# Optimization experiments

Measured on AMD Instinct MI355X. Metric: run time of the kernel, lower is better.

Reference implementation:

```python
import jax, jax.numpy as jnp
import numpy as np
from jax import lax

B, T, IDIM, HDIM = 128, 256, 64, 128
TS, KS, OC1, ANF = 64, 3, 100, 64
S1 = TS - 3 * (KS - 1)   # 58: three VALID ks=3 stride-1 convs
S = S1 * S1              # 3364
HN = 2 * HDIM            # 256 = h_dim * l_dim (l_dim=2)
F = S + HN               # 3620
HID = F // 2             # 1810


def _conv(x, w, b):
    y = lax.conv_general_dilated(x, w, (1, 1), 'VALID',
                                 dimension_numbers=('NCHW', 'OIHW', 'NCHW'))
    return y + b[None, :, None, None]


def _lstm_layer(x, w_ih, w_hh, b_ih, b_hh):
    # x: [B, T, D] -> (outputs [B, T, H], final hidden [B, H]); PyTorch gate order i,f,g,o
    Bn = x.shape[0]
    h0 = jnp.zeros((Bn, HDIM), x.dtype)
    c0 = jnp.zeros((Bn, HDIM), x.dtype)
    def step(carry, xt):
        h, c = carry
        g = xt @ w_ih.T + h @ w_hh.T + b_ih + b_hh
        i, f, gg, o = jnp.split(g, 4, axis=-1)
        c = jax.nn.sigmoid(f) * c + jax.nn.sigmoid(i) * jnp.tanh(gg)
        h = jax.nn.sigmoid(o) * jnp.tanh(c)
        return (h, c), h
    (hT, cT), ys = lax.scan(step, (h0, c0), jnp.swapaxes(x, 0, 1))
    return jnp.swapaxes(ys, 0, 1), hT


def setup_inputs() -> dict:
    key = jax.random.key(0)
    k = jax.random.split(key, 30)
    s = 0.05
    H4 = 4 * HDIM
    return {
        'x1': jax.random.normal(k[0], (B, 3, TS, TS), jnp.float32),
        'x2': jax.random.normal(k[1], (B, T, IDIM), jnp.float32),
        # conv2a/conv2b: two Monte-Carlo weight samples of the same Bayesian conv2 layer
        'conv1_w': jax.random.normal(k[2], (OC1, 3, KS, KS), jnp.float32) * s,
        'conv1_b': jax.random.normal(k[3], (OC1,), jnp.float32) * s,
        'conv2a_w': jax.random.normal(k[4], (OC1, OC1, KS, KS), jnp.float32) * s,
        'conv2a_b': jax.random.normal(k[5], (OC1,), jnp.float32) * s,
        'conv2b_w': jax.random.normal(k[6], (OC1, OC1, KS, KS), jnp.float32) * s,
        'conv2b_b': jax.random.normal(k[7], (OC1,), jnp.float32) * s,
        'w_ih0': jax.random.normal(k[8], (H4, IDIM), jnp.float32) * s,
        'w_hh0': jax.random.normal(k[9], (H4, HDIM), jnp.float32) * s,
        'b_ih0': jax.random.normal(k[10], (H4,), jnp.float32) * s,
        'b_hh0': jax.random.normal(k[11], (H4,), jnp.float32) * s,
        'w_ih1': jax.random.normal(k[12], (H4, HDIM), jnp.float32) * s,
        'w_hh1': jax.random.normal(k[13], (H4, HDIM), jnp.float32) * s,
        'b_ih1': jax.random.normal(k[14], (H4,), jnp.float32) * s,
        'b_hh1': jax.random.normal(k[15], (H4,), jnp.float32) * s,
        'attn1_w': jax.random.normal(k[16], (ANF, F), jnp.float32) * s,
        'attn1_b': jax.random.normal(k[17], (ANF,), jnp.float32) * s,
        'attn2_w': jax.random.normal(k[18], (1, ANF), jnp.float32) * s,
        'attn2_b': jax.random.normal(k[19], (1,), jnp.float32) * s,
        'fc1_w': jax.random.normal(k[20], (HID, F), jnp.float32) * s,
        'fc1_b': jax.random.normal(k[21], (HID,), jnp.float32) * s,
        'fc2_w': jax.random.normal(k[22], (1, HID), jnp.float32) * s,
        'fc2_b': jax.random.normal(k[23], (1,), jnp.float32) * s,
    }


def reference(x1, x2, conv1_w, conv1_b, conv2a_w, conv2a_b, conv2b_w, conv2b_b,
              w_ih0, w_hh0, b_ih0, b_hh0, w_ih1, w_hh1, b_ih1, b_hh1,
              attn1_w, attn1_b, attn2_w, attn2_b, fc1_w, fc1_b, fc2_w, fc2_b):
    Bn = x1.shape[0]
    # CNN branch
    x = jax.nn.relu(_conv(x1, conv1_w, conv1_b))
    x = jax.nn.relu(_conv(x, conv2a_w, conv2a_b))
    x = jax.nn.relu(_conv(x, conv2b_w, conv2b_b))
    xd = x.reshape(Bn, OC1, S)                               # [B, oc1, S]
    # LSTM branch (2 layers, dropout in eval mode = identity)
    y0, h0f = _lstm_layer(x2, w_ih0, w_hh0, b_ih0, b_hh0)
    _, h1f = _lstm_layer(y0, w_ih1, w_hh1, b_ih1, b_hh1)
    hn = jnp.concatenate([h0f, h1f], axis=1)                 # [B, 2*h_dim]
    # Broadcast hidden state across channels (replaces the torch concat loop)
    hn_b = jnp.broadcast_to(hn[:, None, :], (Bn, OC1, HN))
    fused = jnp.concatenate([xd, hn_b], axis=2)              # [B, oc1, F]
    # Attention
    a = jnp.tanh(fused @ attn1_w.T + attn1_b)                # [B, oc1, anf]
    a = a @ attn2_w.T + attn2_b                              # [B, oc1, 1]
    a = jax.nn.softmax(a, axis=1)
    ctx = jnp.einsum('bcs,bco->bso', xd, a).reshape(Bn, S)   # [B, S]
    # Fusion MLP (dropout eval-mode identity)
    m = jnp.concatenate([ctx, hn], axis=1)                   # [B, F]
    h = jax.nn.relu(m @ fc1_w.T + fc1_b)
    return h @ fc2_w.T + fc2_b                               # [B, 1]
```

## Files before the change

kernel.cpp:

```cpp
#include <hip/hip_runtime.h>
#include <hip/hip_bf16.h>
#include <math.h>

#define BB 128
#define TT 256
#define IDIM 64
#define HD 128
#define G4 512
#define OC 100
#define W1 62
#define W2 60
#define W3 58
#define NPX1 (W1*W1)
#define NPX2 (W2*W2)
#define NPX3 (W3*W3)
#define SS NPX3
#define FF (SS + 2*HD)
#define HIDN 1810
#define ANF 64
#define ROWSPLIT 47

typedef __hip_bfloat16 bf16;
typedef _Float16 f16;
typedef __attribute__((ext_vector_type(8))) short bf16x8;
typedef __attribute__((ext_vector_type(4))) short bf16x4;
typedef __attribute__((ext_vector_type(2))) _Float16 half2v;
typedef __attribute__((ext_vector_type(4))) float f32x4;

__device__ __forceinline__ float ldf(const float* p) { return *p; }
__device__ __forceinline__ float ldf(const bf16* p)  { return __bfloat162float(*p); }
__device__ __forceinline__ void  stf(float* p, float v) { *p = v; }
__device__ __forceinline__ void  stf(bf16* p, float v)  { *p = __float2bfloat16(v); }

__device__ __forceinline__ short f2bs(float v) {
    bf16 t = __float2bfloat16(v); short s; __builtin_memcpy(&s, &t, 2); return s;
}
__device__ __forceinline__ float fsig(float x) {
    return __builtin_amdgcn_rcpf(1.f + __expf(-x));
}
__device__ __forceinline__ float ftanh(float x) {
    float t = __expf(-2.f * fabsf(x));
    float r = __builtin_amdgcn_rcpf(1.f + t);
    float m = 1.f - 2.f * t * r;
    return copysignf(m, x);
}
__device__ __forceinline__ float fmix2(unsigned w, unsigned h, float acc) {
    half2v wv, hv;
    __builtin_memcpy(&wv, &w, 4);
    __builtin_memcpy(&hv, &h, 4);
    acc = fmaf((float)wv[0], (float)hv[0], acc);
    acc = fmaf((float)wv[1], (float)hv[1], acc);
    return acc;
}

__device__ __forceinline__ bf16x8 load8(const bf16* p) { return *(const bf16x8*)p; }
__device__ __forceinline__ bf16x8 load8(const float* p) {
    float4 x = *(const float4*)p;
    float4 y = *(const float4*)(p + 4);
    bf16x8 r;
    r[0] = f2bs(x.x); r[1] = f2bs(x.y); r[2] = f2bs(x.z); r[3] = f2bs(x.w);
    r[4] = f2bs(y.x); r[5] = f2bs(y.y); r[6] = f2bs(y.z); r[7] = f2bs(y.w);
    return r;
}

__global__ void zero_kernel(float* o, int n)
{
    int i = blockIdx.x * 256 + threadIdx.x;
    if (i < n) o[i] = 0.f;
}

__device__ __forceinline__ void body_cvt_bf16(const float* __restrict__ s, bf16* __restrict__ d,
                                              int i, int n4)
{
    if (i >= n4) return;
    float4 v = ((const float4*)s)[i];
    bf16x4 o;
    o[0] = f2bs(v.x); o[1] = f2bs(v.y); o[2] = f2bs(v.z); o[3] = f2bs(v.w);
    *(bf16x4*)(d + 4 * (size_t)i) = o;
}
__device__ __forceinline__ void body_cvt_f16(const float* __restrict__ s, f16* __restrict__ d,
                                             int i, int n4)
{
    if (i >= n4) return;
    float4 v = ((const float4*)s)[i];
    f16 o[4] = {(f16)v.x, (f16)v.y, (f16)v.z, (f16)v.w};
    *(uint2*)(d + 4 * (size_t)i) = *(uint2*)o;
}
__device__ __forceinline__ void body_wt(const float* __restrict__ w, bf16* __restrict__ WT, int idx)
{
    if (idx >= 129024) return;
    int i  = idx & 31;
    int oc = (idx >> 5) % 112;
    int ts = idx / (112 * 32);
    int s = ts & 3, t = ts >> 2;
    int ic = s * 32 + i;
    float v = 0.f;
    if (oc < OC && ic < OC) v = w[(oc * OC + ic) * 9 + t];
    WT[idx] = __float2bfloat16(v);
}

__global__ __launch_bounds__(256)
void prep_kernel(const float* __restrict__ x2,   bf16* __restrict__ X2B,
                 const float* __restrict__ whh0, f16*  __restrict__ LWf0,
                 const float* __restrict__ whh1, f16*  __restrict__ LWf1,
                 const float* __restrict__ wih0, bf16* __restrict__ WIH0B,
                 const float* __restrict__ wih1, bf16* __restrict__ WIH1B,
                 const float* __restrict__ a1w,  bf16* __restrict__ A1WB,
                 const float* __restrict__ bih0, const float* __restrict__ bhh0, float* __restrict__ BS0,
                 const float* __restrict__ bih1, const float* __restrict__ bhh1, float* __restrict__ BS1,
                 const float* __restrict__ c2aw, bf16* __restrict__ WTa,
                 const float* __restrict__ c2bw, bf16* __restrict__ WTb)
{
    int bid = blockIdx.x;
    int tid = threadIdx.x;
    if (bid < 2048)      body_cvt_bf16(x2,   X2B,   bid * 256 + tid, 524288);
    else if (bid < 2112) body_cvt_f16 (whh0, LWf0, (bid - 2048) * 256 + tid, 16384);
    else if (bid < 2176) body_cvt_f16 (whh1, LWf1, (bid - 2112) * 256 + tid, 16384);
    else if (bid < 2208) body_cvt_bf16(wih0, WIH0B, (bid - 2176) * 256 + tid, 8192);
    else if (bid < 2272) body_cvt_bf16(wih1, WIH1B, (bid - 2208) * 256 + tid, 16384);
    else if (bid < 2499) body_cvt_bf16(a1w,  A1WB,  (bid - 2272) * 256 + tid, 57920);
    else if (bid < 2500) { BS0[tid] = bih0[tid] + bhh0[tid]; BS0[tid + 256] = bih0[tid + 256] + bhh0[tid + 256]; }
    else if (bid < 2501) { BS1[tid] = bih1[tid] + bhh1[tid]; BS1[tid + 256] = bih1[tid + 256] + bhh1[tid + 256]; }
    else if (bid < 3005) body_wt(c2aw, WTa, (bid - 2501) * 256 + tid);
    else                 body_wt(c2bw, WTb, (bid - 3005) * 256 + tid);
}

__device__ __forceinline__
void conv1_body(const float* __restrict__ x1, const float* __restrict__ wl,
                const float* __restrict__ bl, bf16* __restrict__ out, int b, int py, int t)
{
    int px = py * 256 + t;
    if (px >= NPX1) return;
    int y = px / W1, x = px % W1;
    float in[3][3][3];
    const float* xb = x1 + (size_t)b * 3 * 64 * 64;
#pragma unroll
    for (int ic = 0; ic < 3; ic++)
#pragma unroll
        for (int r = 0; r < 3; r++)
#pragma unroll
            for (int c = 0; c < 3; c++)
                in[ic][r][c] = xb[(ic * 64 + y + r) * 64 + x + c];
    bf16* ob = out + (size_t)b * OC * NPX1 + px;
    for (int oc = 0; oc < OC; ++oc) {
        float acc = bl[oc];
        const float* wp = &wl[oc * 27];
#pragma unroll
        for (int ic = 0; ic < 3; ic++)
#pragma unroll
            for (int r = 0; r < 3; r++)
#pragma unroll
                for (int c = 0; c < 3; c++)
                    acc = fmaf(in[ic][r][c], wp[ic * 9 + r * 3 + c], acc);
        ob[(size_t)oc * NPX1] = __float2bfloat16(fmaxf(acc, 0.f));
    }
}

__global__ __launch_bounds__(256)
void conv1_kernel(const float* __restrict__ x1, const float* __restrict__ w,
                  const float* __restrict__ bias, bf16* __restrict__ out)
{
    __shared__ float wl[2700];
    __shared__ float bl[OC];
    int tid = threadIdx.x;
    for (int i = tid; i < 2700; i += 256) wl[i] = w[i];
    if (tid < OC) bl[tid] = bias[tid];
    __syncthreads();
    conv1_body(x1, wl, bl, out, blockIdx.x, blockIdx.y, tid);
}

__device__ __forceinline__
void conv2_body(const bf16* __restrict__ in, const bf16* __restrict__ WT,
                const float* __restrict__ bias, bf16* __restrict__ out,
                int iw, int ow, int b, int yblk, int tid,
                bf16* __restrict__ il, bf16* __restrict__ wl)
{
    int y0 = yblk * 8;
    int wid = tid >> 6;
    int l = tid & 63;
    int hq = l >> 4;
    int l16 = l & 15;
    int yo = y0 + wid;

    f32x4 acc[7][4];
#pragma unroll
    for (int f = 0; f < 7; f++) {
#pragma unroll
        for (int r = 0; r < 4; r++) {
            int oc = f * 16 + hq * 4 + r;
            float bv = (oc < OC) ? bias[oc] : 0.f;
#pragma unroll
            for (int n = 0; n < 4; n++) acc[f][n][r] = bv;
        }
    }

    const size_t ims = (size_t)iw * iw;
    int icl = tid & 31;
    int t2  = tid >> 5;
    for (int s = 0; s < 4; ++s) {
        __syncthreads();
        int ic = s * 32 + icl;
        bool icok = ic < OC;
        const bf16* ibase = in + (size_t)(b * OC + ic) * ims;
#pragma unroll
        for (int it = 0; it < 6; ++it) {
            int u2 = t2 + it * 16;
            if (u2 < 90) {
                int r = u2 / 9, xb = u2 - r * 9;
                int x8 = xb * 8;
                int yy = y0 + r;
                bf16x8 v = {0, 0, 0, 0, 0, 0, 0, 0};
                if (icok && yy < iw && x8 < iw) {
                    const short* sp = (const short*)(ibase + (size_t)yy * iw + x8);
                    if (x8 + 8 <= iw) {
                        const unsigned* sp32 = (const unsigned*)sp;
#pragma unroll
                        for (int q = 0; q < 4; q++)
                            ((unsigned*)&v)[q] = sp32[q];
                    } else {
                        for (int k = 0; k < 8; k++)
                            if (x8 + k < iw) ((short*)&v)[k] = sp[k];
                    }
                }
                bf16* dst = &il[(r * 72 + x8) * 40 + icl];
#pragma unroll
                for (int k = 0; k < 8; k++)
                    *(short*)&dst[k * 40] = ((short*)&v)[k];
            }
        }
#pragma unroll
        for (int it = 0; it < 8; ++it) {
            int u = tid + it * 512;
            if (u < 4032) {
                int tf = u >> 6; int lp = u & 63;
                int t = tf / 7, f = tf - t * 7;
                int oc = f * 16 + (lp & 15);
                int hq2 = lp >> 4;
                *(bf16x8*)&wl[(size_t)u * 8] =
                    *(const bf16x8*)(WT + (size_t)((t * 4 + s) * 112 + oc) * 32 + hq2 * 8);
            }
        }
        __syncthreads();

#pragma unroll
        for (int ky = 0; ky < 3; ++ky) {
#pragma unroll
            for (int kx = 0; kx < 3; ++kx) {
                int t = ky * 3 + kx;
                bf16x8 a[7];
#pragma unroll
                for (int f = 0; f < 7; f++)
                    a[f] = *(const bf16x8*)&wl[(size_t)((t * 7 + f) * 64 + l) * 8];
                bf16x8 bfr[4];
#pragma unroll
                for (int n = 0; n < 4; n++)
                    bfr[n] = *(const bf16x8*)&il[((wid + ky) * 72 + kx + l16 + n * 16) * 40 + hq * 8];
#pragma unroll
                for (int f = 0; f < 7; f++)
#pragma unroll
                    for (int n = 0; n < 4; n++)
                        acc[f][n] = __builtin_amdgcn_mfma_f32_16x16x32_bf16(
                            a[f], bfr[n], acc[f][n], 0, 0, 0);
            }
        }
    }

    if (yo < ow) {
#pragma unroll
        for (int f = 0; f < 7; f++) {
#pragma unroll
            for (int r = 0; r < 4; r++) {
                int oc = f * 16 + hq * 4 + r;
                if (oc < OC) {
#pragma unroll
                    for (int n = 0; n < 4; n++) {
                        int x = n * 16 + l16;
                        if (x < ow)
                            out[((size_t)(b * OC + oc) * ow + yo) * ow + x] =
                                __float2bfloat16(fmaxf(acc[f][n][r], 0.f));
                    }
                }
            }
        }
    }
}

__global__ __launch_bounds__(512, 1)
void conv2_mfma(const bf16* __restrict__ in, const bf16* __restrict__ WT,
                const float* __restrict__ bias, bf16* __restrict__ out,
                int iw, int ow, int brow0)
{
    __shared__ bf16 il[10 * 72 * 40];
    __shared__ bf16 wl[4032 * 8];
    conv2_body(in, WT, bias, out, iw, ow, brow0 + blockIdx.x, blockIdx.y, threadIdx.x, il, wl);
}

__device__ __forceinline__
void lstm_body(const bf16* __restrict__ G, const f16* __restrict__ LWr,
               bf16* __restrict__ Y, float* __restrict__ HN, int hoff,
               int b, int g, f16* __restrict__ hl, float* __restrict__ ex)
{
    uint4 wv[16];
    const uint4* wp = (const uint4*)(LWr + (size_t)g * HD);
#pragma unroll
    for (int q = 0; q < 16; q++) wv[q] = wp[q];
#pragma unroll
    for (int q = 0; q < 16; q++)
        asm volatile("" : "+v"(wv[q].x), "+v"(wv[q].y), "+v"(wv[q].z), "+v"(wv[q].w));
    float c = 0.f;
    if (g < HD) hl[g] = (f16)0.f;
    __syncthreads();
    const bf16* Gb = G + (size_t)b * TT * G4 + g;
    float gcur = __bfloat162float(Gb[0]);
    for (int t = 0; t < TT; ++t) {
        int tn = (t + 1 < TT) ? t + 1 : t;
        bf16 gnext = Gb[(size_t)tn * G4];
        float a0 = 0.f, a1 = 0.f, a2 = 0.f, a3 = 0.f;
#pragma unroll
        for (int q = 0; q < 16; q++) {
            uint4 hw = *(const uint4*)&hl[q * 8];
            a0 = fmix2(wv[q].x, hw.x, a0);
            a1 = fmix2(wv[q].y, hw.y, a1);
            a2 = fmix2(wv[q].z, hw.z, a2);
            a3 = fmix2(wv[q].w, hw.w, a3);
        }
        float dot = gcur + (a0 + a1) + (a2 + a3);
        float tr;
        if (g < 2 * HD || g >= 3 * HD) tr = fsig(dot);
        else tr = ftanh(dot);
        ex[g] = tr;
        gcur = __bfloat162float(gnext);
        __syncthreads();
        if (g < HD) {
            float iv = ex[g], fv = ex[HD + g], gv = ex[2 * HD + g], ov = ex[3 * HD + g];
            c = fv * c + iv * gv;
            float nh = ov * ftanh(c);
            hl[g] = (f16)nh;
            if (Y) Y[((size_t)b * TT + t) * HD + g] = __float2bfloat16(nh);
            if (t == TT - 1) HN[(size_t)b * 256 + hoff + g] = nh;
        }
        __syncthreads();
    }
}

__global__ __launch_bounds__(512, 1)
void lstm_recur(const bf16* __restrict__ G, const f16* __restrict__ LWr,
                bf16* __restrict__ Y, float* __restrict__ HN, int hoff)
{
    __shared__ __align__(16) f16 hl[HD];
    __shared__ float ex[G4];
    lstm_body(G, LWr, Y, HN, hoff, blockIdx.x, threadIdx.x, hl, ex);
}

__global__ __launch_bounds__(512, 1)
void hybrid_l0c1(const bf16* __restrict__ G, const f16* __restrict__ LWf0,
                 bf16* __restrict__ Y0, float* __restrict__ HN,
                 const float* __restrict__ x1, const float* __restrict__ c1w,
                 const float* __restrict__ c1b, bf16* __restrict__ A1)
{
    __shared__ __align__(16) char smem[11264];
    int bid = blockIdx.x;
    if (bid < BB) {
        lstm_body(G, LWf0, Y0, HN, 0, bid, threadIdx.x,
                  (f16*)smem, (float*)(smem + 512));
    } else {
        float* wl = (float*)smem;
        float* bl = (float*)(smem + 10800);
        int tid = threadIdx.x;
        for (int i = tid; i < 2700; i += 512) wl[i] = c1w[i];
        if (tid < OC) bl[tid] = c1b[tid];
        __syncthreads();
        int v = (bid - BB) * 2 + (tid >> 8);
        conv1_body(x1, wl, bl, A1, v >> 4, v & 15, tid & 255);
    }
}

__global__ __launch_bounds__(512, 1)
void hybrid_l1c2a(const bf16* __restrict__ G, const f16* __restrict__ LWf1,
                  float* __restrict__ HN,
                  const bf16* __restrict__ A1, const bf16* __restrict__ WTa,
                  const float* __restrict__ c2ab, bf16* __restrict__ A2)
{
    __shared__ __align__(16) char smem[122112];
    int bid = blockIdx.x;
    if (bid < BB) {
        lstm_body(G, LWf1, (bf16*)nullptr, HN, HD, bid, threadIdx.x,
                  (f16*)smem, (float*)(smem + 512));
    } else {
        int r = bid - BB;
        conv2_body(A1, WTa, c2ab, A2, W1, W2, ROWSPLIT + (r >> 3), r & 7,
                   threadIdx.x, (bf16*)smem, (bf16*)(smem + 57600));
    }
}

template<typename TB, typename TC, int ACT>
__global__ __launch_bounds__(256)
void gemm_mfma(const bf16* __restrict__ A, int lda,
               const TB* __restrict__ B, int ldb,
               const float* __restrict__ bias,
               TC* __restrict__ C, int ldc,
               int M, int N, int K)
{
    __shared__ bf16 As[64 * 72];
    __shared__ bf16 Bs[64 * 72];
    int tid = threadIdx.x;
    int l = tid & 63, wid = tid >> 6;
    int l16 = l & 15, h = l >> 4;
    int m0 = blockIdx.x * 64, n0 = blockIdx.y * 64;
    f32x4 acc[4];
#pragma unroll
    for (int nb = 0; nb < 4; nb++) acc[nb] = (f32x4){0.f, 0.f, 0.f, 0.f};

    int rs = tid >> 3;
    int kc = (tid & 7) * 8;

    for (int k0 = 0; k0 < K; k0 += 64) {
        int kr = K - k0;
#pragma unroll
        for (int half = 0; half < 2; half++) {
            int rr = rs + half * 32;
            bf16x8 av = {0, 0, 0, 0, 0, 0, 0, 0};
            int m = m0 + rr;
            if (m < M) {
                const short* src = (const short*)(A + (size_t)m * lda + k0 + kc);
                if (kc + 8 <= kr) av = *(const bf16x8*)src;
                else if (kc < kr) {
                    for (int j = 0; j < 8; j++) if (kc + j < kr) ((short*)&av)[j] = src[j];
                }
            }
            *(bf16x8*)&As[rr * 72 + kc] = av;
            bf16x8 bv = {0, 0, 0, 0, 0, 0, 0, 0};
            int n = n0 + rr;
            if (n < N) {
                const TB* src = B + (size_t)n * ldb + k0 + kc;
                if (kc + 8 <= kr) bv = load8(src);
                else if (kc < kr) {
                    for (int j = 0; j < 8; j++) if (kc + j < kr) ((short*)&bv)[j] = f2bs(ldf(src + j));
                }
            }
            *(bf16x8*)&Bs[rr * 72 + kc] = bv;
        }
        __syncthreads();
#pragma unroll
        for (int kk = 0; kk < 2; kk++) {
            bf16x8 af = *(const bf16x8*)&As[(wid * 16 + l16) * 72 + kk * 32 + h * 8];
#pragma unroll
            for (int nb = 0; nb < 4; nb++) {
                bf16x8 bfr = *(const bf16x8*)&Bs[(nb * 16 + l16) * 72 + kk * 32 + h * 8];
                acc[nb] = __builtin_amdgcn_mfma_f32_16x16x32_bf16(af, bfr, acc[nb], 0, 0, 0);
            }
        }
        __syncthreads();
    }
#pragma unroll
    for (int nb = 0; nb < 4; nb++) {
        int col = n0 + nb * 16 + l16;
        if (col >= N) continue;
        float bv = bias ? bias[col] : 0.f;
#pragma unroll
        for (int reg = 0; reg < 4; reg++) {
            int row = m0 + wid * 16 + h * 4 + reg;
            if (row < M) {
                float v = acc[nb][reg] + bv;
                if (ACT == 1) v = fmaxf(v, 0.f);
                stf(&C[(size_t)row * ldc + col], v);
            }
        }
    }
}

template<typename TA, typename TC, int BM, int BN, int BK, int TM, int TN, int ACT>
__global__ __launch_bounds__((BM / TM) * (BN / TN))
void gemm_tn(const TA* __restrict__ A, int lda,
             const float* __restrict__ Bmat, int ldb,
             const float* __restrict__ bias,
             TC* __restrict__ C, int ldc,
             int M, int N, int K)
{
    constexpr int TX = BN / TN;
    constexpr int TY = BM / TM;
    constexpr int NT = TX * TY;
    __shared__ float As[BK][BM + 1];
    __shared__ float Bs[BK][BN + 1];
    int tid = threadIdx.x;
    int tx = tid % TX, ty = tid / TX;
    int m0 = blockIdx.x * BM, n0 = blockIdx.y * BN;
    float acc[TM][TN] = {};
    for (int k0 = 0; k0 < K; k0 += BK) {
        for (int idx = tid; idx < BM * BK; idx += NT) {
            int i = idx / BK, j = idx % BK;
            int m = m0 + i, k = k0 + j;
            As[j][i] = (m < M && k < K) ? ldf(&A[(size_t)m * lda + k]) : 0.f;
        }
        for (int idx = tid; idx < BN * BK; idx += NT) {
            int i = idx / BK, j = idx % BK;
            int n = n0 + i, k = k0 + j;
            Bs[j][i] = (n < N && k < K) ? Bmat[(size_t)n * ldb + k] : 0.f;
        }
        __syncthreads();
#pragma unroll
        for (int k = 0; k < BK; ++k) {
            float av[TM], bv[TN];
#pragma unroll
            for (int i = 0; i < TM; i++) av[i] = As[k][ty * TM + i];
#pragma unroll
            for (int j = 0; j < TN; j++) bv[j] = Bs[k][tx * TN + j];
#pragma unroll
            for (int i = 0; i < TM; i++)
#pragma unroll
                for (int j = 0; j < TN; j++)
                    acc[i][j] += av[i] * bv[j];
        }
        __syncthreads();
    }
#pragma unroll
    for (int i = 0; i < TM; i++) {
        int m = m0 + ty * TM + i;
        if (m >= M) continue;
#pragma unroll
        for (int j = 0; j < TN; j++) {
            int n = n0 + tx * TN + j;
            if (n >= N) continue;
            float v = acc[i][j] + (bias ? bias[n] : 0.f);
            if (ACT == 1) v = fmaxf(v, 0.f);
            stf(&C[(size_t)m * ldc + n], v);
        }
    }
}

__global__ __launch_bounds__(128)
void attn_softmax(const float* __restrict__ T1,
                  const float* __restrict__ HB,
                  const float* __restrict__ a2w,
                  const float* __restrict__ a2b,
                  float* __restrict__ ATT)
{
    __shared__ float hbl[ANF];
    __shared__ float awl[ANF];
    __shared__ float red[128];
    int b = blockIdx.x, tid = threadIdx.x;
    if (tid < ANF) { hbl[tid] = HB[b * ANF + tid]; awl[tid] = a2w[tid]; }
    __syncthreads();
    float lg = -1e30f;
    if (tid < OC) {
        const float* tp = T1 + (size_t)(b * OC + tid) * ANF;
        float s = 0.f;
#pragma unroll 4
        for (int j = 0; j < ANF; j++) s += ftanh(tp[j] + hbl[j]) * awl[j];
        lg = s + a2b[0];
    }
    red[tid] = lg; __syncthreads();
    for (int st = 64; st > 0; st >>= 1) { if (tid < st) red[tid] = fmaxf(red[tid], red[tid + st]); __syncthreads(); }
    float mx = red[0]; __syncthreads();
    float e = (tid < OC) ? __expf(lg - mx) : 0.f;
    red[tid] = e; __syncthreads();
    for (int st = 64; st > 0; st >>= 1) { if (tid < st) red[tid] += red[tid + st]; __syncthreads(); }
    if (tid < OC) ATT[b * OC + tid] = e / red[0];
}

__global__ __launch_bounds__(256)
void ctx_concat(const bf16* __restrict__ XD,
                const float* __restrict__ ATT,
                const float* __restrict__ HN,
                bf16* __restrict__ M)
{
    __shared__ float al[OC];
    int b = blockIdx.x;
    int tid = threadIdx.x;
    if (tid < OC) al[tid] = ATT[b * OC + tid];
    __syncthreads();
    int s = blockIdx.y * 256 + tid;
    if (s < SS) {
        const bf16* xp = XD + (size_t)b * OC * SS + s;
        float acc = 0.f;
#pragma unroll 4
        for (int c = 0; c < OC; c++) acc = fmaf(__bfloat162float(xp[(size_t)c * SS]), al[c], acc);
        M[(size_t)b * FF + s] = __float2bfloat16(acc);
    } else if (s < FF) {
        M[(size_t)b * FF + s] = __float2bfloat16(HN[b * 256 + (s - SS)]);
    }
}

__global__ __launch_bounds__(256)
void fc2_kernel(const float* __restrict__ H1, const float* __restrict__ w,
                const float* __restrict__ bias, float* __restrict__ out)
{
    int tid = threadIdx.x;
    int lane = tid & 63, wid = tid >> 6;
    int b = blockIdx.x * 4 + wid;
    float acc = 0.f;
    for (int j = lane; j < HIDN; j += 64) acc = fmaf(H1[(size_t)b * HIDN + j], w[j], acc);
#pragma unroll
    for (int off = 32; off > 0; off >>= 1) acc += __shfl_down(acc, off, 64);
    if (lane == 0) out[b] = acc + bias[0];
}

extern "C" void kernel_launch(void* const* d_in, const int* in_sizes, int n_in,
                              void* d_out, int out_size, void* d_ws, size_t ws_size,
                              hipStream_t stream)
{
    const float* x1   = (const float*)d_in[0];
    const float* x2   = (const float*)d_in[1];
    const float* c1w  = (const float*)d_in[2];
    const float* c1b  = (const float*)d_in[3];
    const float* c2aw = (const float*)d_in[4];
    const float* c2ab = (const float*)d_in[5];
    const float* c2bw = (const float*)d_in[6];
    const float* c2bb = (const float*)d_in[7];
    const float* wih0 = (const float*)d_in[8];
    const float* whh0 = (const float*)d_in[9];
    const float* bih0 = (const float*)d_in[10];
    const float* bhh0 = (const float*)d_in[11];
    const float* wih1 = (const float*)d_in[12];
    const float* whh1 = (const float*)d_in[13];
    const float* bih1 = (const float*)d_in[14];
    const float* bhh1 = (const float*)d_in[15];
    const float* a1w  = (const float*)d_in[16];
    const float* a1b  = (const float*)d_in[17];
    const float* a2w  = (const float*)d_in[18];
    const float* a2b  = (const float*)d_in[19];
    const float* f1w  = (const float*)d_in[20];
    const float* f1b  = (const float*)d_in[21];
    const float* f2w  = (const float*)d_in[22];
    const float* f2b  = (const float*)d_in[23];
    float* out = (float*)d_out;

    char* base = (char*)d_ws;
    bf16* G0    = (bf16*)(base + 0);
    bf16* Y0    = (bf16*)(base + 33554432);
    bf16* G1    = G0;
    bf16* X2B   = (bf16*)(base + 41943040);
    bf16* WIH0B = (bf16*)(base + 46137344);
    bf16* WIH1B = (bf16*)(base + 46202880);
    const size_t LSTM_END = 46333952;

    int nb = 0; size_t ov = 0;
    for (int cand = BB; cand >= 32; cand >>= 1) {
        size_t cnn = (size_t)cand * OC * (NPX1 + NPX2) * 2;
        size_t o = cnn > LSTM_END ? cnn : LSTM_END;
        size_t q = o + 2048 + 2048 + 131072 + 32768
                 + (size_t)cand * OC * 64 * 4
                 + (((size_t)cand * OC * 4 + 255) & ~(size_t)255)
                 + 926720 + 926720 + 258048 + 258048 + 463360
                 + 262144;
        if (ws_size >= q) { nb = cand; ov = o; break; }
    }
    if (nb == 0) {
        zero_kernel<<<1, 128, 0, stream>>>(out, out_size);
        return;
    }
    bf16* A1c;
    bf16* A2c;
    if (nb == BB) {
        A2c = (bf16*)(base + 0);
        A1c = (bf16*)(base + (size_t)BB * OC * NPX2 * 2);
    } else {
        A1c = (bf16*)(base + 0);
        A2c = (bf16*)(base + (size_t)nb * OC * NPX1 * 2);
    }
    bf16* XDc = A1c;
    size_t p = ov;
    float* BS0  = (float*)(base + p); p += 2048;
    float* BS1  = (float*)(base + p); p += 2048;
    float* HN   = (float*)(base + p); p += 131072;
    float* HB   = (float*)(base + p); p += 32768;
    float* T1c  = (float*)(base + p); p += (size_t)nb * OC * 64 * 4;
    float* ATTc = (float*)(base + p); p += ((size_t)nb * OC * 4 + 255) & ~(size_t)255;
    bf16*  MBb  = (bf16*)(base + p); p += 926720;
    float* H1   = (float*)(base + p); p += 926720;
    bf16* WTa   = (bf16*)(base + p); p += 258048;
    bf16* WTb   = (bf16*)(base + p); p += 258048;
    bf16* A1WB  = (bf16*)(base + p); p += 463360;
    f16*  LWf0  = (f16*)(base + p); p += 131072;
    f16*  LWf1  = (f16*)(base + p); p += 131072;

    prep_kernel<<<3509, 256, 0, stream>>>(
        x2, X2B, whh0, LWf0, whh1, LWf1, wih0, WIH0B, wih1, WIH1B, a1w, A1WB,
        bih0, bhh0, BS0, bih1, bhh1, BS1, c2aw, WTa, c2bw, WTb);

    gemm_mfma<bf16, bf16, 0><<<dim3(512, 8), 256, 0, stream>>>(
        X2B, IDIM, WIH0B, IDIM, BS0, G0, G4, BB * TT, G4, IDIM);

    if (nb == BB) {
        hybrid_l0c1<<<BB + BB * 8, 512, 0, stream>>>(
            G0, LWf0, Y0, HN, x1, c1w, c1b, A1c);
        gemm_mfma<bf16, bf16, 0><<<dim3(512, 8), 256, 0, stream>>>(
            Y0, HD, WIH1B, HD, BS1, G1, G4, BB * TT, G4, HD);
        hybrid_l1c2a<<<BB + (BB - ROWSPLIT) * 8, 512, 0, stream>>>(
            G1, LWf1, HN, A1c, WTa, c2ab, A2c);
        conv2_mfma<<<dim3(ROWSPLIT, 8), 512, 0, stream>>>(A1c, WTa, c2ab, A2c, W1, W2, 0);
        conv2_mfma<<<dim3(BB, 8), 512, 0, stream>>>(A2c, WTb, c2bb, XDc, W2, W3, 0);
        gemm_tn<float, float, 32, 32, 16, 2, 2, 0><<<dim3(4, 2), 256, 0, stream>>>(
            HN, 256, a1w + SS, FF, a1b, HB, ANF, BB, ANF, 256);
        gemm_mfma<bf16, float, 0><<<dim3(BB * OC / 64, 1), 256, 0, stream>>>(
            XDc, SS, A1WB, FF, nullptr, T1c, ANF, BB * OC, ANF, SS);
        attn_softmax<<<BB, 128, 0, stream>>>(T1c, HB, a2w, a2b, ATTc);
        ctx_concat<<<dim3(BB, 15), 256, 0, stream>>>(XDc, ATTc, HN, MBb);
    } else {
        lstm_recur<<<BB, 512, 0, stream>>>(G0, LWf0, Y0, HN, 0);
        gemm_mfma<bf16, bf16, 0><<<dim3(512, 8), 256, 0, stream>>>(
            Y0, HD, WIH1B, HD, BS1, G1, G4, BB * TT, G4, HD);
        lstm_recur<<<BB, 512, 0, stream>>>(G1, LWf1, (bf16*)nullptr, HN, HD);
        gemm_tn<float, float, 32, 32, 16, 2, 2, 0><<<dim3(4, 2), 256, 0, stream>>>(
            HN, 256, a1w + SS, FF, a1b, HB, ANF, BB, ANF, 256);
        for (int c0 = 0; c0 < BB; c0 += nb) {
            conv1_kernel<<<dim3(nb, 16), 256, 0, stream>>>(
                x1 + (size_t)c0 * 3 * 64 * 64, c1w, c1b, A1c);
            conv2_mfma<<<dim3(nb, 8), 512, 0, stream>>>(A1c, WTa, c2ab, A2c, W1, W2, 0);
            conv2_mfma<<<dim3(nb, 8), 512, 0, stream>>>(A2c, WTb, c2bb, XDc, W2, W3, 0);
            gemm_mfma<bf16, float, 0><<<dim3(nb * OC / 64, 1), 256, 0, stream>>>(
                XDc, SS, A1WB, FF, nullptr, T1c, ANF, nb * OC, ANF, SS);
            attn_softmax<<<nb, 128, 0, stream>>>(T1c, HB + (size_t)c0 * ANF, a2w, a2b, ATTc);
            ctx_concat<<<dim3(nb, 15), 256, 0, stream>>>(
                XDc, ATTc, HN + (size_t)c0 * 256, MBb + (size_t)c0 * FF);
        }
    }

    gemm_mfma<float, float, 1><<<dim3(2, 29), 256, 0, stream>>>(
        MBb, FF, f1w, FF, f1b, H1, HIDN, BB, HIDN, FF);
    fc2_kernel<<<BB / 4, 256, 0, stream>>>(H1, f2w, f2b, out);
}
```

Measured before the change: 1.058 ms.

## Restructure LSTM recurrence to one thread per hidden unit with LDS-resident gate weights

The LSTM step now uses 128 active threads per block, each computing all four gates for its hidden unit. The i-gate weights stay in registers and the f, g and o weights sit in padded LDS. A double-buffered h vector leaves one barrier per timestep instead of two, and the gate exchange through shared memory is gone. The conv2a work carried inside the hybrid layer-1 kernel is shrunk, and the remaining batches run in an extra conv2 launch. In exchange, 384 of 512 threads sit idle, each active thread does four times the dot-product work with heavy LDS weight reads, and the hybrid kernels need much more shared memory.

```diff
diff --git a/kernel.cpp b/kernel.cpp
--- a/kernel.cpp
+++ b/kernel.cpp
@@ -19,6 +19,7 @@
 #define HIDN 1810
 #define ANF 64
 #define ROWSPLIT 47
+#define HEND 104
 
 typedef __hip_bfloat16 bf16;
 typedef _Float16 f16;
@@ -296,48 +297,66 @@
 }
 
 __device__ __forceinline__
-void lstm_body(const bf16* __restrict__ G, const f16* __restrict__ LWr,
-               bf16* __restrict__ Y, float* __restrict__ HN, int hoff,
-               int b, int g, f16* __restrict__ hl, float* __restrict__ ex)
-{
+void lstm_v2_body(const bf16* __restrict__ G, const f16* __restrict__ LWr,
+                  bf16* __restrict__ Y, float* __restrict__ HN, int hoff,
+                  int b, int tid, f16* __restrict__ Wl ,
+                  f16* __restrict__ hb )
+{
+    for (int idx = tid; idx < 384 * 16; idx += 512) {
+        int row = idx >> 4, q = idx & 15;
+        *(uint4*)&Wl[row * 132 + q * 8] =
+            *(const uint4*)(LWr + (size_t)(HD + row) * HD + q * 8);
+    }
+    int u = tid;
+    bool act = (u < HD);
     uint4 wv[16];
-    const uint4* wp = (const uint4*)(LWr + (size_t)g * HD);
+    const uint4* wp = (const uint4*)(LWr + (size_t)(act ? u : 0) * HD);
 #pragma unroll
     for (int q = 0; q < 16; q++) wv[q] = wp[q];
 #pragma unroll
     for (int q = 0; q < 16; q++)
         asm volatile("" : "+v"(wv[q].x), "+v"(wv[q].y), "+v"(wv[q].z), "+v"(wv[q].w));
+    if (act) hb[u] = (f16)0.f;
     float c = 0.f;
-    if (g < HD) hl[g] = (f16)0.f;
+    const bf16* Gb = G + (size_t)b * TT * G4 + (act ? u : 0);
+    bf16 gx0 = Gb[0], gx1 = Gb[HD], gx2 = Gb[2 * HD], gx3 = Gb[3 * HD];
+    const f16* Wf = Wl + (size_t)u * 132;
+    const f16* Wg = Wl + (size_t)(HD + u) * 132;
+    const f16* Wo = Wl + (size_t)(2 * HD + u) * 132;
+    bool hasY = (Y != nullptr);
     __syncthreads();
-    const bf16* Gb = G + (size_t)b * TT * G4 + g;
-    float gcur = __bfloat162float(Gb[0]);
     for (int t = 0; t < TT; ++t) {
-        int tn = (t + 1 < TT) ? t + 1 : t;
-        bf16 gnext = Gb[(size_t)tn * G4];
-        float a0 = 0.f, a1 = 0.f, a2 = 0.f, a3 = 0.f;
-#pragma unroll
-        for (int q = 0; q < 16; q++) {
-            uint4 hw = *(const uint4*)&hl[q * 8];
-            a0 = fmix2(wv[q].x, hw.x, a0);
-            a1 = fmix2(wv[q].y, hw.y, a1);
-            a2 = fmix2(wv[q].z, hw.z, a2);
-            a3 = fmix2(wv[q].w, hw.w, a3);
-        }
-        float dot = gcur + (a0 + a1) + (a2 + a3);
-        float tr;
-        if (g < 2 * HD || g >= 3 * HD) tr = fsig(dot);
-        else tr = ftanh(dot);
-        ex[g] = tr;
-        gcur = __bfloat162float(gnext);
-        __syncthreads();
-        if (g < HD) {
-            float iv = ex[g], fv = ex[HD + g], gv = ex[2 * HD + g], ov = ex[3 * HD + g];
+        if (act) {
+            const f16* hr = hb + (t & 1) * HD;
+            int tn = (t + 1 < TT) ? t + 1 : t;
+            const bf16* Gn = Gb + (size_t)tn * G4;
+            bf16 gn0 = Gn[0], gn1 = Gn[HD], gn2 = Gn[2 * HD], gn3 = Gn[3 * HD];
+            float d0 = 0.f, d1 = 0.f, d2 = 0.f, d3 = 0.f;
+#pragma unroll
+            for (int q = 0; q < 16; q++) {
+                uint4 hw = *(const uint4*)&hr[q * 8];
+                uint4 wf = *(const uint4*)&Wf[q * 8];
+                uint4 wg = *(const uint4*)&Wg[q * 8];
+                uint4 wo = *(const uint4*)&Wo[q * 8];
+                d0 = fmix2(wv[q].x, hw.x, d0); d0 = fmix2(wv[q].y, hw.y, d0);
+                d0 = fmix2(wv[q].z, hw.z, d0); d0 = fmix2(wv[q].w, hw.w, d0);
+                d1 = fmix2(wf.x, hw.x, d1); d1 = fmix2(wf.y, hw.y, d1);
+                d1 = fmix2(wf.z, hw.z, d1); d1 = fmix2(wf.w, hw.w, d1);
+                d2 = fmix2(wg.x, hw.x, d2); d2 = fmix2(wg.y, hw.y, d2);
+                d2 = fmix2(wg.z, hw.z, d2); d2 = fmix2(wg.w, hw.w, d2);
+                d3 = fmix2(wo.x, hw.x, d3); d3 = fmix2(wo.y, hw.y, d3);
+                d3 = fmix2(wo.z, hw.z, d3); d3 = fmix2(wo.w, hw.w, d3);
+            }
+            float iv = fsig(d0 + __bfloat162float(gx0));
+            float fv = fsig(d1 + __bfloat162float(gx1));
+            float gv = ftanh(d2 + __bfloat162float(gx2));
+            float ov = fsig(d3 + __bfloat162float(gx3));
             c = fv * c + iv * gv;
             float nh = ov * ftanh(c);
-            hl[g] = (f16)nh;
-            if (Y) Y[((size_t)b * TT + t) * HD + g] = __float2bfloat16(nh);
-            if (t == TT - 1) HN[(size_t)b * 256 + hoff + g] = nh;
+            hb[((t + 1) & 1) * HD + u] = (f16)nh;
+            if (hasY) Y[((size_t)b * TT + t) * HD + u] = __float2bfloat16(nh);
+            if (t == TT - 1) HN[(size_t)b * 256 + hoff + u] = nh;
+            gx0 = gn0; gx1 = gn1; gx2 = gn2; gx3 = gn3;
         }
         __syncthreads();
     }
@@ -347,9 +366,9 @@
 void lstm_recur(const bf16* __restrict__ G, const f16* __restrict__ LWr,
                 bf16* __restrict__ Y, float* __restrict__ HN, int hoff)
 {
-    __shared__ __align__(16) f16 hl[HD];
-    __shared__ float ex[G4];
-    lstm_body(G, LWr, Y, HN, hoff, blockIdx.x, threadIdx.x, hl, ex);
+    __shared__ __align__(16) f16 Wl[384 * 132];
+    __shared__ __align__(16) f16 hb[2 * HD];
+    lstm_v2_body(G, LWr, Y, HN, hoff, blockIdx.x, threadIdx.x, Wl, hb);
 }
 
 __global__ __launch_bounds__(512, 1)
@@ -358,11 +377,11 @@
                  const float* __restrict__ x1, const float* __restrict__ c1w,
                  const float* __restrict__ c1b, bf16* __restrict__ A1)
 {
-    __shared__ __align__(16) char smem[11264];
+    __shared__ __align__(16) char smem[102400];
     int bid = blockIdx.x;
     if (bid < BB) {
-        lstm_body(G, LWf0, Y0, HN, 0, bid, threadIdx.x,
-                  (f16*)smem, (float*)(smem + 512));
+        lstm_v2_body(G, LWf0, Y0, HN, 0, bid, threadIdx.x,
+                     (f16*)smem, (f16*)(smem + 101376));
     } else {
         float* wl = (float*)smem;
         float* bl = (float*)(smem + 10800);
@@ -384,8 +403,8 @@
     __shared__ __align__(16) char smem[122112];
     int bid = blockIdx.x;
     if (bid < BB) {
-        lstm_body(G, LWf1, (bf16*)nullptr, HN, HD, bid, threadIdx.x,
-                  (f16*)smem, (float*)(smem + 512));
+        lstm_v2_body(G, LWf1, (bf16*)nullptr, HN, HD, bid, threadIdx.x,
+                     (f16*)smem, (f16*)(smem + 101376));
     } else {
         int r = bid - BB;
         conv2_body(A1, WTa, c2ab, A2, W1, W2, ROWSPLIT + (r >> 3), r & 7,
@@ -686,9 +705,10 @@
             G0, LWf0, Y0, HN, x1, c1w, c1b, A1c);
         gemm_mfma<bf16, bf16, 0><<<dim3(512, 8), 256, 0, stream>>>(
             Y0, HD, WIH1B, HD, BS1, G1, G4, BB * TT, G4, HD);
-        hybrid_l1c2a<<<BB + (BB - ROWSPLIT) * 8, 512, 0, stream>>>(
+        hybrid_l1c2a<<<BB + (HEND - ROWSPLIT) * 8, 512, 0, stream>>>(
             G1, LWf1, HN, A1c, WTa, c2ab, A2c);
         conv2_mfma<<<dim3(ROWSPLIT, 8), 512, 0, stream>>>(A1c, WTa, c2ab, A2c, W1, W2, 0);
+        conv2_mfma<<<dim3(BB - HEND, 8), 512, 0, stream>>>(A1c, WTa, c2ab, A2c, W1, W2, HEND);
         conv2_mfma<<<dim3(BB, 8), 512, 0, stream>>>(A2c, WTb, c2bb, XDc, W2, W3, 0);
         gemm_tn<float, float, 32, 32, 16, 2, 2, 0><<<dim3(4, 2), 256, 0, stream>>>(
             HN, 256, a1w + SS, FF, a1b, HB, ANF, BB, ANF, 256);
```

New measurement: 2.140 ms. 102% more time.

## Fuse weight prep into the G0 GEMM, fold the hidden projection into softmax, rebalance the conv2a split

Applied to the files above, without the earlier changes.

Moves the wih1, attention-weight and conv2 weight conversions out of the prep kernel and into a new kernel that also runs the layer-0 input GEMM, so those conversions overlap with the GEMM blocks. It drops the separate small gemm_tn launch for the hidden-state attention projection and computes that 64x256 dot product inside attn_softmax per batch row. It also narrows the conv2a rows done in the hybrid LSTM-layer-1 kernel and adds a separate conv2_mfma launch for the remaining rows. This saves launches and idle tail time, but adds a serial per-thread 256-long dot product reading strided a1w in softmax, plus one extra conv launch.

```diff
diff --git a/kernel.cpp b/kernel.cpp
--- a/kernel.cpp
+++ b/kernel.cpp
@@ -19,6 +19,7 @@
 #define HIDN 1810
 #define ANF 64
 #define ROWSPLIT 47
+#define HEND 112
 
 typedef __hip_bfloat16 bf16;
 typedef _Float16 f16;
@@ -104,12 +105,8 @@
                  const float* __restrict__ whh0, f16*  __restrict__ LWf0,
                  const float* __restrict__ whh1, f16*  __restrict__ LWf1,
                  const float* __restrict__ wih0, bf16* __restrict__ WIH0B,
-                 const float* __restrict__ wih1, bf16* __restrict__ WIH1B,
-                 const float* __restrict__ a1w,  bf16* __restrict__ A1WB,
                  const float* __restrict__ bih0, const float* __restrict__ bhh0, float* __restrict__ BS0,
-                 const float* __restrict__ bih1, const float* __restrict__ bhh1, float* __restrict__ BS1,
-                 const float* __restrict__ c2aw, bf16* __restrict__ WTa,
-                 const float* __restrict__ c2bw, bf16* __restrict__ WTb)
+                 const float* __restrict__ bih1, const float* __restrict__ bhh1, float* __restrict__ BS1)
 {
     int bid = blockIdx.x;
     int tid = threadIdx.x;
@@ -117,12 +114,8 @@
     else if (bid < 2112) body_cvt_f16 (whh0, LWf0, (bid - 2048) * 256 + tid, 16384);
     else if (bid < 2176) body_cvt_f16 (whh1, LWf1, (bid - 2112) * 256 + tid, 16384);
     else if (bid < 2208) body_cvt_bf16(wih0, WIH0B, (bid - 2176) * 256 + tid, 8192);
-    else if (bid < 2272) body_cvt_bf16(wih1, WIH1B, (bid - 2208) * 256 + tid, 16384);
-    else if (bid < 2499) body_cvt_bf16(a1w,  A1WB,  (bid - 2272) * 256 + tid, 57920);
-    else if (bid < 2500) { BS0[tid] = bih0[tid] + bhh0[tid]; BS0[tid + 256] = bih0[tid + 256] + bhh0[tid + 256]; }
-    else if (bid < 2501) { BS1[tid] = bih1[tid] + bhh1[tid]; BS1[tid + 256] = bih1[tid + 256] + bhh1[tid + 256]; }
-    else if (bid < 3005) body_wt(c2aw, WTa, (bid - 2501) * 256 + tid);
-    else                 body_wt(c2bw, WTb, (bid - 3005) * 256 + tid);
+    else if (bid < 2209) { BS0[tid] = bih0[tid] + bhh0[tid]; BS0[tid + 256] = bih0[tid + 256] + bhh0[tid + 256]; }
+    else                 { BS1[tid] = bih1[tid] + bhh1[tid]; BS1[tid + 256] = bih1[tid + 256] + bhh1[tid + 256]; }
 }
 
 __device__ __forceinline__
@@ -394,19 +387,16 @@
 }
 
 template<typename TB, typename TC, int ACT>
-__global__ __launch_bounds__(256)
-void gemm_mfma(const bf16* __restrict__ A, int lda,
+__device__ __forceinline__
+void gemm_body(const bf16* __restrict__ A, int lda,
                const TB* __restrict__ B, int ldb,
                const float* __restrict__ bias,
                TC* __restrict__ C, int ldc,
-               int M, int N, int K)
-{
-    __shared__ bf16 As[64 * 72];
-    __shared__ bf16 Bs[64 * 72];
-    int tid = threadIdx.x;
+               int M, int N, int K, int m0, int n0, int tid,
+               bf16* __restrict__ As, bf16* __restrict__ Bs)
+{
     int l = tid & 63, wid = tid >> 6;
     int l16 = l & 15, h = l >> 4;
-    int m0 = blockIdx.x * 64, n0 = blockIdx.y * 64;
     f32x4 acc[4];
 #pragma unroll
     for (int nb = 0; nb < 4; nb++) acc[nb] = (f32x4){0.f, 0.f, 0.f, 0.f};
@@ -469,77 +459,70 @@
     }
 }
 
-template<typename TA, typename TC, int BM, int BN, int BK, int TM, int TN, int ACT>
-__global__ __launch_bounds__((BM / TM) * (BN / TN))
-void gemm_tn(const TA* __restrict__ A, int lda,
-             const float* __restrict__ Bmat, int ldb,
-             const float* __restrict__ bias,
-             TC* __restrict__ C, int ldc,
-             int M, int N, int K)
-{
-    constexpr int TX = BN / TN;
-    constexpr int TY = BM / TM;
-    constexpr int NT = TX * TY;
-    __shared__ float As[BK][BM + 1];
-    __shared__ float Bs[BK][BN + 1];
+template<typename TB, typename TC, int ACT>
+__global__ __launch_bounds__(256)
+void gemm_mfma(const bf16* __restrict__ A, int lda,
+               const TB* __restrict__ B, int ldb,
+               const float* __restrict__ bias,
+               TC* __restrict__ C, int ldc,
+               int M, int N, int K)
+{
+    __shared__ bf16 As[64 * 72];
+    __shared__ bf16 Bs[64 * 72];
+    gemm_body<TB, TC, ACT>(A, lda, B, ldb, bias, C, ldc, M, N, K,
+                           blockIdx.x * 64, blockIdx.y * 64, threadIdx.x, As, Bs);
+}
+
+__global__ __launch_bounds__(256)
+void g0prep(const bf16* __restrict__ X2B, const bf16* __restrict__ WIH0B,
+            const float* __restrict__ BS0, bf16* __restrict__ G0,
+            const float* __restrict__ wih1, bf16* __restrict__ WIH1B,
+            const float* __restrict__ a1w,  bf16* __restrict__ A1WB,
+            const float* __restrict__ c2aw, bf16* __restrict__ WTa,
+            const float* __restrict__ c2bw, bf16* __restrict__ WTb)
+{
+    int bid = blockIdx.x;
     int tid = threadIdx.x;
-    int tx = tid % TX, ty = tid / TX;
-    int m0 = blockIdx.x * BM, n0 = blockIdx.y * BN;
-    float acc[TM][TN] = {};
-    for (int k0 = 0; k0 < K; k0 += BK) {
-        for (int idx = tid; idx < BM * BK; idx += NT) {
-            int i = idx / BK, j = idx % BK;
-            int m = m0 + i, k = k0 + j;
-            As[j][i] = (m < M && k < K) ? ldf(&A[(size_t)m * lda + k]) : 0.f;
-        }
-        for (int idx = tid; idx < BN * BK; idx += NT) {
-            int i = idx / BK, j = idx % BK;
-            int n = n0 + i, k = k0 + j;
-            Bs[j][i] = (n < N && k < K) ? Bmat[(size_t)n * ldb + k] : 0.f;
-        }
-        __syncthreads();
-#pragma unroll
-        for (int k = 0; k < BK; ++k) {
-            float av[TM], bv[TN];
-#pragma unroll
-            for (int i = 0; i < TM; i++) av[i] = As[k][ty * TM + i];
-#pragma unroll
-            for (int j = 0; j < TN; j++) bv[j] = Bs[k][tx * TN + j];
-#pragma unroll
-            for (int i = 0; i < TM; i++)
-#pragma unroll
-                for (int j = 0; j < TN; j++)
-                    acc[i][j] += av[i] * bv[j];
-        }
-        __syncthreads();
-    }
-#pragma unroll
-    for (int i = 0; i < TM; i++) {
-        int m = m0 + ty * TM + i;
-        if (m >= M) continue;
-#pragma unroll
-        for (int j = 0; j < TN; j++) {
-            int n = n0 + tx * TN + j;
-            if (n >= N) continue;
-            float v = acc[i][j] + (bias ? bias[n] : 0.f);
-            if (ACT == 1) v = fmaxf(v, 0.f);
-            stf(&C[(size_t)m * ldc + n], v);
-        }
+    if (bid < 4096) {
+        __shared__ bf16 As[64 * 72];
+        __shared__ bf16 Bs[64 * 72];
+        gemm_body<bf16, bf16, 0>(X2B, IDIM, WIH0B, IDIM, BS0, G0, G4,
+                                 BB * TT, G4, IDIM,
+                                 (bid & 511) * 64, (bid >> 9) * 64, tid, As, Bs);
+    } else {
+        int r = bid - 4096;
+        if (r < 64)       body_cvt_bf16(wih1, WIH1B, r * 256 + tid, 16384);
+        else if (r < 291) body_cvt_bf16(a1w,  A1WB, (r - 64) * 256 + tid, 57920);
+        else if (r < 795) body_wt(c2aw, WTa, (r - 291) * 256 + tid);
+        else              body_wt(c2bw, WTb, (r - 795) * 256 + tid);
     }
 }
 
 __global__ __launch_bounds__(128)
 void attn_softmax(const float* __restrict__ T1,
-                  const float* __restrict__ HB,
+                  const float* __restrict__ HNb,
+                  const float* __restrict__ a1w,
+                  const float* __restrict__ a1b,
                   const float* __restrict__ a2w,
                   const float* __restrict__ a2b,
                   float* __restrict__ ATT)
 {
+    __shared__ float hnl[256];
     __shared__ float hbl[ANF];
     __shared__ float awl[ANF];
     __shared__ float red[128];
     int b = blockIdx.x, tid = threadIdx.x;
-    if (tid < ANF) { hbl[tid] = HB[b * ANF + tid]; awl[tid] = a2w[tid]; }
+    hnl[tid]       = HNb[b * 256 + tid];
+    hnl[tid + 128] = HNb[b * 256 + 128 + tid];
+    if (tid < ANF) awl[tid] = a2w[tid];
+    __syncthreads();
+    if (tid < ANF) {
+        const float* ap = a1w + (size_t)tid * FF + SS;
+        float s = a1b[tid];
+#pragma unroll 4
+        for (int k = 0; k < 256; k++) s = fmaf(hnl[k], ap[k], s);
+        hbl[tid] = s;
+    }
     __syncthreads();
     float lg = -1e30f;
     if (tid < OC) {
@@ -638,7 +621,7 @@
     for (int cand = BB; cand >= 32; cand >>= 1) {
         size_t cnn = (size_t)cand * OC * (NPX1 + NPX2) * 2;
         size_t o = cnn > LSTM_END ? cnn : LSTM_END;
-        size_t q = o + 2048 + 2048 + 131072 + 32768
+        size_t q = o + 2048 + 2048 + 131072
                  + (size_t)cand * OC * 64 * 4
                  + (((size_t)cand * OC * 4 + 255) & ~(size_t)255)
                  + 926720 + 926720 + 258048 + 258048 + 463360
@@ -663,7 +646,6 @@
     float* BS0  = (float*)(base + p); p += 2048;
     float* BS1  = (float*)(base + p); p += 2048;
     float* HN   = (float*)(base + p); p += 131072;
-    float* HB   = (float*)(base + p); p += 32768;
     float* T1c  = (float*)(base + p); p += (size_t)nb * OC * 64 * 4;
     float* ATTc = (float*)(base + p); p += ((size_t)nb * OC * 4 + 255) & ~(size_t)255;
     bf16*  MBb  = (bf16*)(base + p); p += 926720;
@@ -674,35 +656,32 @@
     f16*  LWf0  = (f16*)(base + p); p += 131072;
     f16*  LWf1  = (f16*)(base + p); p += 131072;
 
-    prep_kernel<<<3509, 256, 0, stream>>>(
-        x2, X2B, whh0, LWf0, whh1, LWf1, wih0, WIH0B, wih1, WIH1B, a1w, A1WB,
-        bih0, bhh0, BS0, bih1, bhh1, BS1, c2aw, WTa, c2bw, WTb);
-
-    gemm_mfma<bf16, bf16, 0><<<dim3(512, 8), 256, 0, stream>>>(
-        X2B, IDIM, WIH0B, IDIM, BS0, G0, G4, BB * TT, G4, IDIM);
+    prep_kernel<<<2210, 256, 0, stream>>>(
+        x2, X2B, whh0, LWf0, whh1, LWf1, wih0, WIH0B,
+        bih0, bhh0, BS0, bih1, bhh1, BS1);
+
+    g0prep<<<5395, 256, 0, stream>>>(
+        X2B, WIH0B, BS0, G0, wih1, WIH1B, a1w, A1WB, c2aw, WTa, c2bw, WTb);
 
     if (nb == BB) {
         hybrid_l0c1<<<BB + BB * 8, 512, 0, stream>>>(
             G0, LWf0, Y0, HN, x1, c1w, c1b, A1c);
         gemm_mfma<bf16, bf16, 0><<<dim3(512, 8), 256, 0, stream>>>(
             Y0, HD, WIH1B, HD, BS1, G1, G4, BB * TT, G4, HD);
-        hybrid_l1c2a<<<BB + (BB - ROWSPLIT) * 8, 512, 0, stream>>>(
+        hybrid_l1c2a<<<BB + (HEND - ROWSPLIT) * 8, 512, 0, stream>>>(
             G1, LWf1, HN, A1c, WTa, c2ab, A2c);
         conv2_mfma<<<dim3(ROWSPLIT, 8), 512, 0, stream>>>(A1c, WTa, c2ab, A2c, W1, W2, 0);
+        conv2_mfma<<<dim3(BB - HEND, 8), 512, 0, stream>>>(A1c, WTa, c2ab, A2c, W1, W2, HEND);
         conv2_mfma<<<dim3(BB, 8), 512, 0, stream>>>(A2c, WTb, c2bb, XDc, W2, W3, 0);
-        gemm_tn<float, float, 32, 32, 16, 2, 2, 0><<<dim3(4, 2), 256, 0, stream>>>(
-            HN, 256, a1w + SS, FF, a1b, HB, ANF, BB, ANF, 256);
         gemm_mfma<bf16, float, 0><<<dim3(BB * OC / 64, 1), 256, 0, stream>>>(
             XDc, SS, A1WB, FF, nullptr, T1c, ANF, BB * OC, ANF, SS);
-        attn_softmax<<<BB, 128, 0, stream>>>(T1c, HB, a2w, a2b, ATTc);
+        attn_softmax<<<BB, 128, 0, stream>>>(T1c, HN, a1w, a1b, a2w, a2b, ATTc);
         ctx_concat<<<dim3(BB, 15), 256, 0, stream>>>(XDc, ATTc, HN, MBb);
     } else {
         lstm_recur<<<BB, 512, 0, stream>>>(G0, LWf0, Y0, HN, 0);
         gemm_mfma<bf16, bf16, 0><<<dim3(512, 8), 256, 0, stream>>>(
             Y0, HD, WIH1B, HD, BS1, G1, G4, BB * TT, G4, HD);
         lstm_recur<<<BB, 512, 0, stream>>>(G1, LWf1, (bf16*)nullptr, HN, HD);
-        gemm_tn<float, float, 32, 32, 16, 2, 2, 0><<<dim3(4, 2), 256, 0, stream>>>(
-            HN, 256, a1w + SS, FF, a1b, HB, ANF, BB, ANF, 256);
         for (int c0 = 0; c0 < BB; c0 += nb) {
             conv1_kernel<<<dim3(nb, 16), 256, 0, stream>>>(
                 x1 + (size_t)c0 * 3 * 64 * 64, c1w, c1b, A1c);
@@ -710,7 +689,8 @@
             conv2_mfma<<<dim3(nb, 8), 512, 0, stream>>>(A2c, WTb, c2bb, XDc, W2, W3, 0);
             gemm_mfma<bf16, float, 0><<<dim3(nb * OC / 64, 1), 256, 0, stream>>>(
                 XDc, SS, A1WB, FF, nullptr, T1c, ANF, nb * OC, ANF, SS);
-            attn_softmax<<<nb, 128, 0, stream>>>(T1c, HB + (size_t)c0 * ANF, a2w, a2b, ATTc);
+            attn_softmax<<<nb, 128, 0, stream>>>(
+                T1c, HN + (size_t)c0 * 256, a1w, a1b, a2w, a2b, ATTc);
             ctx_concat<<<dim3(nb, 15), 256, 0, stream>>>(
                 XDc, ATTc, HN + (size_t)c0 * 256, MBb + (size_t)c0 * FF);
         }
```

Result: no change. 1.064 ms (+0.6%).
